# Kernel optimization log

Hardware: AMD Instinct MI355X
Metric: run time of the kernel (lower is better)

## Reference

```python
import jax, jax.numpy as jnp
import numpy as np

N_SRC0, N_FTRS, N_HID, N_CLS = 200000, 128, 1500, 64
E0, E1 = 1600000, 500000
RES0, RES1 = 50000, 10000


def sage_conv(x, src, tgt, res_size, W_root, W_neigh, b):
    # mean aggregation of neighbor (source) features onto the first res_size target nodes
    msg = x[src]                                              # [E, F] gather
    summed = jax.ops.segment_sum(msg, tgt, num_segments=res_size)   # [res, F]
    cnt = jax.ops.segment_sum(jnp.ones((src.shape[0],), x.dtype), tgt, num_segments=res_size)
    mean = summed / jnp.maximum(cnt, 1.0)[:, None]
    return x[:res_size] @ W_root + mean @ W_neigh + b


def setup_inputs() -> dict:
    key = jax.random.key(0)
    ks = jax.random.split(key, 12)
    x = jax.random.normal(ks[0], (N_SRC0, N_FTRS), dtype=jnp.float32)
    edge_src0 = jax.random.randint(ks[1], (E0,), 0, N_SRC0)
    edge_tgt0 = jax.random.randint(ks[2], (E0,), 0, RES0)
    edge_src1 = jax.random.randint(ks[3], (E1,), 0, RES0)
    edge_tgt1 = jax.random.randint(ks[4], (E1,), 0, RES1)
    s1 = 1.0 / np.sqrt(N_FTRS)
    s2 = 1.0 / np.sqrt(N_HID)
    W1_root = jax.random.uniform(ks[5], (N_FTRS, N_HID), jnp.float32, -s1, s1)
    W1_neigh = jax.random.uniform(ks[6], (N_FTRS, N_HID), jnp.float32, -s1, s1)
    b1 = jax.random.uniform(ks[7], (N_HID,), jnp.float32, -s1, s1)
    W2_root = jax.random.uniform(ks[8], (N_HID, N_CLS), jnp.float32, -s2, s2)
    W2_neigh = jax.random.uniform(ks[9], (N_HID, N_CLS), jnp.float32, -s2, s2)
    b2 = jax.random.uniform(ks[10], (N_CLS,), jnp.float32, -s2, s2)
    return {
        "x": x,
        "W1_root": W1_root, "W1_neigh": W1_neigh, "b1": b1,
        "W2_root": W2_root, "W2_neigh": W2_neigh, "b2": b2,
        "edge_src0": edge_src0, "edge_tgt0": edge_tgt0,
        "edge_src1": edge_src1, "edge_tgt1": edge_tgt1,
        "res0": RES0, "res1": RES1,
    }


def reference(x, W1_root, W1_neigh, b1, W2_root, W2_neigh, b2,
              edge_src0, edge_tgt0, edge_src1, edge_tgt1, res0, res1):
    h = sage_conv(x, edge_src0, edge_tgt0, res0, W1_root, W1_neigh, b1)  # [res0, H]
    h = jax.nn.relu(h)
    # dropout p=0.5 is identity in eval mode
    out = sage_conv(h, edge_src1, edge_tgt1, res1, W2_root, W2_neigh, b2)  # [res1, C]
    return jax.nn.log_softmax(out, axis=1)
```

## Files before the change

kernel.cpp:

```cpp
#include <hip/hip_runtime.h>
#include <hip/hip_bf16.h>
#include <cstdint>
#include <cstddef>

#define NSRC   200000
#define NF     128
#define NHID   1500
#define NHIDP  1536
#define NCLS   64
#define E0N    1600000
#define E1N    500000
#define RES0   50000
#define RES1   10000

#define CH     4096
#define NCH0   ((E0N + CH - 1) / CH)
#define NCH1   ((E1N + CH - 1) / CH)
#define NB0    ((RES0 + 255) / 256)
#define NB1    ((RES1 + 255) / 256)

#define PREP_BLOCKS  ((256 * NHIDP + 128 * NHIDP + NHIDP + 255) / 256)
#define COPYX_BLOCKS ((NSRC * NF) / (256 * 8))

typedef __bf16 bf16x8 __attribute__((ext_vector_type(8)));
typedef float  f32x4  __attribute__((ext_vector_type(4)));
typedef unsigned short u16x8 __attribute__((ext_vector_type(8)));
typedef unsigned int u32;
typedef unsigned long long u64;

__device__ __forceinline__ unsigned short f2bf(float f) {
    union { float f; unsigned u; } v; v.f = f;
    unsigned r = v.u + 0x7fffu + ((v.u >> 16) & 1u);
    return (unsigned short)(r >> 16);
}
__device__ __forceinline__ float bf2f(unsigned short b) {
    union { u32 u; float f; } v; v.u = ((u32)b) << 16;
    return v.f;
}

__device__ __forceinline__ u32 cvt_pk_bf16(float lo, float hi) {
    u32 r;
    asm("v_cvt_pk_bf16_f32 %0, %1, %2" : "=v"(r) : "v"(lo), "v"(hi));
    return r;
}

__device__ __forceinline__ void lds_dma16(const void* g, void* lds) {
    __builtin_amdgcn_global_load_lds(
        (const __attribute__((address_space(1))) unsigned int*)g,
        (__attribute__((address_space(3))) unsigned int*)lds, 16, 0, 0);
}

__device__ __forceinline__ void raw_barrier() {
    __asm__ volatile("s_barrier" ::: "memory");
}
__device__ __forceinline__ void wait_vm8() {
    __asm__ volatile("s_waitcnt vmcnt(8)" ::: "memory");
}
__device__ __forceinline__ void wait_vm4() {
    __asm__ volatile("s_waitcnt vmcnt(4)" ::: "memory");
}
__device__ __forceinline__ void wait_vm0() {
    __asm__ volatile("s_waitcnt vmcnt(0)" ::: "memory");
}

__device__ __forceinline__ void p1a_body(const int* __restrict__ tgt, int n,
                                         int nb, u32* __restrict__ H, int c) {
    __shared__ u32 lhist[256];
    int tid = threadIdx.x;
    lhist[tid] = 0;
    __syncthreads();
#pragma unroll
    for (int it = 0; it < CH / 256; ++it) {
        int i = c * CH + it * 256 + tid;
        if (i < n) atomicAdd(&lhist[((u32)tgt[i]) >> 8], 1u);
    }
    __syncthreads();
    if (tid < nb) H[c * nb + tid] = lhist[tid];
}

__global__ __launch_bounds__(256) void setup_kernel(
        const float* __restrict__ x, unsigned short* __restrict__ xbf,
        const float* __restrict__ W1r, const float* __restrict__ W1n,
        const float* __restrict__ b1,
        const float* __restrict__ W2r, const float* __restrict__ W2n,
        unsigned short* __restrict__ WcatT, unsigned short* __restrict__ W2f,
        float* __restrict__ b1e,
        const int* __restrict__ t0, const int* __restrict__ t1,
        u32* __restrict__ H1, u32* __restrict__ H2) {
    int bid = blockIdx.x;
    if (bid < PREP_BLOCKS) {
        int id = bid * 256 + threadIdx.x;
        if (id < 256 * NHIDP) {
            int n = id >> 8, k = id & 255;
            float v = 0.f;
            if (n < NHID) v = (k < NF) ? W1r[k * NHID + n] : W1n[(k - NF) * NHID + n];
            WcatT[n * 256 + k] = f2bf(v);
        } else {
            int id2 = id - 256 * NHIDP;
            if (id2 < 128 * NHIDP) {
                int n = id2 / NHIDP, k = id2 % NHIDP;
                float v = 0.f;
                if (k < NHID) v = (n < 64) ? W2n[k * 64 + n] : W2r[k * 64 + (n - 64)];
                int j = k >> 7, w = k & 127;
                int kk = w >> 5, r = w & 31;
                int hi = r >> 4, qd = (r >> 2) & 3, e = r & 3;
                W2f[(((size_t)(j * 4 + kk) * 128 + n) * 32) + qd * 8 + hi * 4 + e] = f2bf(v);
            } else {
                int c = id2 - 128 * NHIDP;
                if (c < NHIDP) b1e[c] = (c < NHID) ? b1[c] : 0.f;
            }
        }
    } else if (bid < PREP_BLOCKS + COPYX_BLOCKS) {
        size_t i = ((size_t)(bid - PREP_BLOCKS) * 256 + threadIdx.x) * 8;
        const float4* s = (const float4*)(x + i);
        float4 a = s[0], b = s[1];
        u16x8 o;
        o[0] = f2bf(a.x); o[1] = f2bf(a.y); o[2] = f2bf(a.z); o[3] = f2bf(a.w);
        o[4] = f2bf(b.x); o[5] = f2bf(b.y); o[6] = f2bf(b.z); o[7] = f2bf(b.w);
        *(u16x8*)(xbf + i) = o;
    } else {
        int c = bid - (PREP_BLOCKS + COPYX_BLOCKS);
        if (c < NCH0) p1a_body(t0, E0N, NB0, H1, c);
        else          p1a_body(t1, E1N, NB1, H2, c - NCH0);
    }
}

__device__ __forceinline__ void bscan_body(const u32* __restrict__ H,
                                           int nch, int nb, int b,
                                           u32* __restrict__ base_rel,
                                           u32* __restrict__ Bsum) {
    __shared__ u32 part[512];
    int t = threadIdx.x;
    part[t] = (t < nch) ? H[t * nb + b] : 0u;
    __syncthreads();
    for (int d = 1; d < 512; d <<= 1) {
        u32 v = part[t];
        u32 add = (t >= d) ? part[t - d] : 0u;
        __syncthreads();
        part[t] = v + add;
        __syncthreads();
    }
    if (t < nch) base_rel[t * nb + b] = (t == 0) ? 0u : part[t - 1];
    if (t == 0) Bsum[b] = part[nch - 1];
}

__global__ __launch_bounds__(512) void bscan_both_kernel(
        const u32* __restrict__ H1, u32* __restrict__ base1, u32* __restrict__ Bsum1,
        const u32* __restrict__ H2, u32* __restrict__ base2, u32* __restrict__ Bsum2) {
    int b = blockIdx.x;
    if (b < NB0) bscan_body(H1, NCH0, NB0, b, base1, Bsum1);
    else         bscan_body(H2, NCH1, NB1, b - NB0, base2, Bsum2);
}

__global__ __launch_bounds__(256) void boff_kernel(const u32* __restrict__ Bsum1,
                                                   u32* __restrict__ boff1, int nb1,
                                                   const u32* __restrict__ Bsum2,
                                                   u32* __restrict__ boff2, int nb2) {
    const u32* B = blockIdx.x ? Bsum2 : Bsum1;
    u32* O = blockIdx.x ? boff2 : boff1;
    int nb = blockIdx.x ? nb2 : nb1;
    __shared__ u32 part[256];
    int t = threadIdx.x;
    part[t] = (t < nb) ? B[t] : 0u;
    __syncthreads();
    for (int d = 1; d < 256; d <<= 1) {
        u32 v = part[t];
        u32 add = (t >= d) ? part[t - d] : 0u;
        __syncthreads();
        part[t] = v + add;
        __syncthreads();
    }
    if (t < nb) O[t] = (t == 0) ? 0u : part[t - 1];
}

__device__ __forceinline__ void p1b_body(const int* __restrict__ src,
                                         const int* __restrict__ tgt, int n,
                                         int nb, const u32* __restrict__ base_rel,
                                         const u32* __restrict__ boff,
                                         u64* __restrict__ bucketed, int c) {
    __shared__ u32 lcur[256];
    __shared__ u32 lbase[256];
    int tid = threadIdx.x;
    lcur[tid] = 0;
    if (tid < nb) lbase[tid] = base_rel[c * nb + tid] + boff[tid];
    __syncthreads();
#pragma unroll
    for (int it = 0; it < CH / 256; ++it) {
        int i = c * CH + it * 256 + tid;
        if (i < n) {
            u32 t = (u32)tgt[i];
            u32 s = (u32)src[i];
            u32 b = t >> 8;
            u32 r = atomicAdd(&lcur[b], 1u);
            bucketed[lbase[b] + r] = ((u64)t << 32) | (u64)s;
        }
    }
}

__global__ __launch_bounds__(256) void p1b_both_kernel(
        const int* __restrict__ s0, const int* __restrict__ t0,
        const u32* __restrict__ base1, const u32* __restrict__ boff1,
        u64* __restrict__ bkt1,
        const int* __restrict__ s1, const int* __restrict__ t1,
        const u32* __restrict__ base2, const u32* __restrict__ boff2,
        u64* __restrict__ bkt2) {
    int b = blockIdx.x;
    if (b < NCH0) p1b_body(s0, t0, E0N, NB0, base1, boff1, bkt1, b);
    else          p1b_body(s1, t1, E1N, NB1, base2, boff2, bkt2, b - NCH0);
}

__device__ __forceinline__ void p2_body(const u64* __restrict__ bucketed,
                                        const u32* __restrict__ boff,
                                        int nb, int res, int etot,
                                        int* __restrict__ csr,
                                        u32* __restrict__ off_out,
                                        u32* __restrict__ cnt_out, int b) {
    __shared__ u32 lhist[256];
    __shared__ u32 part[256];
    __shared__ u32 cur[256];
    int tid = threadIdx.x;
    u32 start = boff[b];
    u32 end = (b == nb - 1) ? (u32)etot : boff[b + 1];
    u32 count = end - start;
    if (tid < 256) lhist[tid] = 0;
    __syncthreads();
    for (u32 i = tid; i < count; i += 1024) {
        u32 t = (u32)(bucketed[start + i] >> 32);
        atomicAdd(&lhist[t & 255u], 1u);
    }
    __syncthreads();
    if (tid < 256) part[tid] = lhist[tid];
    __syncthreads();
    for (int d = 1; d < 256; d <<= 1) {
        u32 v = (tid < 256) ? part[tid] : 0u;
        u32 add = (tid >= d && tid < 256) ? part[tid - d] : 0u;
        __syncthreads();
        if (tid < 256) part[tid] = v + add;
        __syncthreads();
    }
    if (tid < 256) {
        u32 excl = (tid == 0) ? 0u : part[tid - 1];
        cur[tid] = excl;
        int tg = (b << 8) + tid;
        if (tg < res) {
            off_out[tg] = start + excl;
            cnt_out[tg] = lhist[tid];
        }
    }
    __syncthreads();
    for (u32 i = tid; i < count; i += 1024) {
        u64 pr = bucketed[start + i];
        u32 lt = ((u32)(pr >> 32)) & 255u;
        u32 r = atomicAdd(&cur[lt], 1u);
        csr[start + r] = (int)(u32)pr;
    }
}

__global__ __launch_bounds__(1024) void p2_both_kernel(
        const u64* __restrict__ bkt1, const u32* __restrict__ boff1,
        int* __restrict__ csr1, u32* __restrict__ off1, u32* __restrict__ cnt1,
        const u64* __restrict__ bkt2, const u32* __restrict__ boff2,
        int* __restrict__ csr2, u32* __restrict__ off2, u32* __restrict__ cnt2) {
    int b = blockIdx.x;
    if (b < NB0) p2_body(bkt1, boff1, NB0, RES0, E0N, csr1, off1, cnt1, b);
    else         p2_body(bkt2, boff2, NB1, RES1, E1N, csr2, off2, cnt2, b - NB0);
}

__global__ __launch_bounds__(256) void agg1_csr_kernel(
        const unsigned short* __restrict__ xbf, const int* __restrict__ csr,
        const u32* __restrict__ off, const u32* __restrict__ cnt,
        unsigned short* __restrict__ mean1) {
    int row = blockIdx.x * 4 + (threadIdx.x >> 6);
    int lane = threadIdx.x & 63;
    if (row >= RES0) return;
    int q = lane >> 4, c16 = lane & 15;
    u32 base = off[row], deg = cnt[row];
    float acc[8] = {};
    u32 e = 0;
    for (; e + 16 <= deg; e += 16) {
        int s0 = csr[base + e + q];
        int s1 = csr[base + e + 4 + q];
        int s2 = csr[base + e + 8 + q];
        int s3 = csr[base + e + 12 + q];
        u16x8 v0 = *(const u16x8*)(xbf + (size_t)s0 * NF + c16 * 8);
        u16x8 v1 = *(const u16x8*)(xbf + (size_t)s1 * NF + c16 * 8);
        u16x8 v2 = *(const u16x8*)(xbf + (size_t)s2 * NF + c16 * 8);
        u16x8 v3 = *(const u16x8*)(xbf + (size_t)s3 * NF + c16 * 8);
#pragma unroll
        for (int i = 0; i < 8; ++i)
            acc[i] += (bf2f(v0[i]) + bf2f(v1[i])) + (bf2f(v2[i]) + bf2f(v3[i]));
    }
    for (; e + 8 <= deg; e += 8) {
        int s0 = csr[base + e + q];
        int s1 = csr[base + e + 4 + q];
        u16x8 v0 = *(const u16x8*)(xbf + (size_t)s0 * NF + c16 * 8);
        u16x8 v1 = *(const u16x8*)(xbf + (size_t)s1 * NF + c16 * 8);
#pragma unroll
        for (int i = 0; i < 8; ++i) acc[i] += bf2f(v0[i]) + bf2f(v1[i]);
    }
    for (; e + 4 <= deg; e += 4) {
        int s0 = csr[base + e + q];
        u16x8 v0 = *(const u16x8*)(xbf + (size_t)s0 * NF + c16 * 8);
#pragma unroll
        for (int i = 0; i < 8; ++i) acc[i] += bf2f(v0[i]);
    }
    if (e < deg) {
        bool valid = (e + q) < deg;
        int s0 = csr[base + (valid ? e + q : e)];
        u16x8 v0 = *(const u16x8*)(xbf + (size_t)s0 * NF + c16 * 8);
        if (valid) {
#pragma unroll
            for (int i = 0; i < 8; ++i) acc[i] += bf2f(v0[i]);
        }
    }
#pragma unroll
    for (int i = 0; i < 8; ++i) {
        acc[i] += __shfl_xor(acc[i], 32, 64);
        acc[i] += __shfl_xor(acc[i], 16, 64);
    }
    if (q == 0) {
        float inv = 1.0f / fmaxf((float)deg, 1.0f);
        u16x8 o;
#pragma unroll
        for (int i = 0; i < 8; ++i) o[i] = f2bf(acc[i] * inv);
        *(u16x8*)(mean1 + (size_t)row * NF + c16 * 8) = o;
    }
}

__device__ __forceinline__ void stage_chunk(
        const unsigned short* __restrict__ xbf, const unsigned short* __restrict__ mean1,
        const unsigned short* __restrict__ WcatT, int m0, int j, int kt,
        unsigned short* As, unsigned short* Bs, int wid, int lane) {
    int ksel = kt * 32;
    const unsigned short* srcA = (ksel < 128)
        ? xbf + (size_t)m0 * NF + ksel
        : mean1 + (size_t)m0 * NF + (ksel - 128);
#pragma unroll
    for (int ci = 0; ci < 2; ++ci) {
        int cb = ci * 256 + wid * 64;
        int chunk = cb + lane;
        int n = chunk >> 2, kc = (chunk & 3) ^ (n & 3);
        lds_dma16(srcA + (size_t)n * NF + kc * 8, &As[cb * 8]);
    }
    const unsigned short* srcB = WcatT + (size_t)(j * 128) * 256 + ksel;
#pragma unroll
    for (int ci = 0; ci < 2; ++ci) {
        int cb = ci * 256 + wid * 64;
        int chunk = cb + lane;
        int n = chunk >> 2, kc = (chunk & 3) ^ (n & 3);
        lds_dma16(srcB + (size_t)n * 256 + kc * 8, &Bs[cb * 8]);
    }
}

__global__ __launch_bounds__(256, 2) void fused_gemm_kernel(
        const unsigned short* __restrict__ xbf, const unsigned short* __restrict__ mean1,
        const unsigned short* __restrict__ WcatT, const float* __restrict__ b1e,
        const unsigned short* __restrict__ W2f,
        unsigned short* __restrict__ pnbf, float* __restrict__ root64) {
    __shared__ __align__(16) unsigned short As[4][128 * 32];
    __shared__ __align__(16) unsigned short Bs[4][128 * 32];

    int m0 = blockIdx.x * 128;
    int tid = threadIdx.x;
    int lane = tid & 63, wid = tid >> 6;
    int wm = wid;
    int quad = lane >> 4, l15 = lane & 15;
    const int csw = (quad ^ (l15 & 3)) * 8;

    f32x4 pacc[2][8] = {};

    stage_chunk(xbf, mean1, WcatT, m0, 0, 0, As[0], Bs[0], wid, lane);
    stage_chunk(xbf, mean1, WcatT, m0, 0, 1, As[1], Bs[1], wid, lane);
    stage_chunk(xbf, mean1, WcatT, m0, 0, 2, As[2], Bs[2], wid, lane);

#pragma unroll 1
    for (int jj = 0; jj < 12; ++jj) {
        const int j = jj;
        f32x4 hacc[2][8] = {};
#pragma unroll
        for (int kt = 0; kt < 8; ++kt) {
            const int g = jj * 8 + kt;
            if (g <= 93) wait_vm8();
            else if (g == 94) wait_vm4();
            else wait_vm0();
            raw_barrier();
            if (g + 3 < 96) {
                int g3 = g + 3;
                stage_chunk(xbf, mean1, WcatT, m0, g3 >> 3, g3 & 7,
                            As[g3 & 3], Bs[g3 & 3], wid, lane);
            }
            const unsigned short* Asb = As[g & 3];
            const unsigned short* Bsb = Bs[g & 3];
            bf16x8 a[2], b[8];
#pragma unroll
            for (int mi = 0; mi < 2; ++mi)
                a[mi] = *(const bf16x8*)(&Asb[(wm * 32 + mi * 16 + l15) * 32 + csw]);
#pragma unroll
            for (int ni = 0; ni < 8; ++ni)
                b[ni] = *(const bf16x8*)(&Bsb[(ni * 16 + l15) * 32 + csw]);
            __builtin_amdgcn_s_setprio(1);
#pragma unroll
            for (int mi = 0; mi < 2; ++mi)
#pragma unroll
                for (int ni = 0; ni < 8; ++ni)
                    hacc[mi][ni] = __builtin_amdgcn_mfma_f32_16x16x32_bf16(b[ni], a[mi], hacc[mi][ni], 0, 0, 0);
            __builtin_amdgcn_s_setprio(0);
        }

        u32 a2w[2][4][4];
#pragma unroll
        for (int ni = 0; ni < 8; ++ni) {
            float4 bv = *(const float4*)(b1e + j * 128 + ni * 16 + quad * 4);
#pragma unroll
            for (int mi = 0; mi < 2; ++mi) {
                f32x4 h = hacc[mi][ni];
                float h0 = fmaxf(h[0] + bv.x, 0.f);
                float h1 = fmaxf(h[1] + bv.y, 0.f);
                float h2 = fmaxf(h[2] + bv.z, 0.f);
                float h3 = fmaxf(h[3] + bv.w, 0.f);
                a2w[mi][ni >> 1][(ni & 1) * 2 + 0] = cvt_pk_bf16(h0, h1);
                a2w[mi][ni >> 1][(ni & 1) * 2 + 1] = cvt_pk_bf16(h2, h3);
            }
        }
        __builtin_amdgcn_s_setprio(1);
#pragma unroll
        for (int kk = 0; kk < 4; ++kk) {
            union U { u32 w[4]; bf16x8 v; uint4 q; };
            U A2[2];
#pragma unroll
            for (int mi = 0; mi < 2; ++mi)
#pragma unroll
                for (int w = 0; w < 4; ++w) A2[mi].w[w] = a2w[mi][kk][w];
            const unsigned short* wp =
                W2f + ((size_t)(j * 4 + kk) * 128) * 32 + (size_t)quad * 8;
#pragma unroll
            for (int ni2 = 0; ni2 < 8; ++ni2) {
                U B2;
                B2.q = *(const uint4*)(wp + (size_t)(ni2 * 16 + l15) * 32);
#pragma unroll
                for (int mi = 0; mi < 2; ++mi)
                    pacc[mi][ni2] = __builtin_amdgcn_mfma_f32_16x16x32_bf16(B2.v, A2[mi].v, pacc[mi][ni2], 0, 0, 0);
            }
        }
        __builtin_amdgcn_s_setprio(0);
    }

#pragma unroll
    for (int mi = 0; mi < 2; ++mi) {
        int gr = m0 + wm * 32 + mi * 16 + l15;
        if (gr < RES0) {
#pragma unroll
            for (int ni2 = 0; ni2 < 8; ++ni2) {
                f32x4 s = pacc[mi][ni2];
                if (ni2 < 4) {
                    uint2 o;
                    o.x = (u32)f2bf(s[0]) | ((u32)f2bf(s[1]) << 16);
                    o.y = (u32)f2bf(s[2]) | ((u32)f2bf(s[3]) << 16);
                    *(uint2*)(pnbf + (size_t)gr * 64 + ni2 * 16 + quad * 4) = o;
                } else if (gr < RES1) {
                    *(f32x4*)(root64 + (size_t)gr * 64 + (ni2 - 4) * 16 + quad * 4) = s;
                }
            }
        }
    }
}

__global__ __launch_bounds__(256) void final_csr_kernel(
        const unsigned short* __restrict__ pnbf, const float* __restrict__ root64,
        const int* __restrict__ csr, const u32* __restrict__ off,
        const u32* __restrict__ cnt, const float* __restrict__ b2,
        float* __restrict__ out) {
    int row = blockIdx.x * 4 + (threadIdx.x >> 6);
    int lane = threadIdx.x & 63;
    if (row >= RES1) return;
    int es = lane >> 3, c8 = lane & 7;
    u32 base = off[row], deg = cnt[row];
    float acc[8] = {};
    u32 e = 0;
    for (; e + 8 <= deg; e += 8) {
        int s = csr[base + e + es];
        u16x8 v = *(const u16x8*)(pnbf + (size_t)s * 64 + c8 * 8);
#pragma unroll
        for (int i = 0; i < 8; ++i) acc[i] += bf2f(v[i]);
    }
    if (e < deg) {
        bool valid = (e + es) < deg;
        int s = csr[base + (valid ? e + es : e)];
        u16x8 v = *(const u16x8*)(pnbf + (size_t)s * 64 + c8 * 8);
        if (valid) {
#pragma unroll
            for (int i = 0; i < 8; ++i) acc[i] += bf2f(v[i]);
        }
    }
#pragma unroll
    for (int i = 0; i < 8; ++i) {
        acc[i] += __shfl_xor(acc[i], 32, 64);
        acc[i] += __shfl_xor(acc[i], 16, 64);
        acc[i] += __shfl_xor(acc[i], 8, 64);
    }
    float inv = 1.0f / fmaxf((float)deg, 1.0f);
    float v[8];
    const float* rp = root64 + (size_t)row * 64 + c8 * 8;
#pragma unroll
    for (int i = 0; i < 8; ++i) v[i] = rp[i] + acc[i] * inv + b2[c8 * 8 + i];
    float m = v[0];
#pragma unroll
    for (int i = 1; i < 8; ++i) m = fmaxf(m, v[i]);
    m = fmaxf(m, __shfl_xor(m, 1, 64));
    m = fmaxf(m, __shfl_xor(m, 2, 64));
    m = fmaxf(m, __shfl_xor(m, 4, 64));
    float s = 0.f;
#pragma unroll
    for (int i = 0; i < 8; ++i) s += expf(v[i] - m);
    s += __shfl_xor(s, 1, 64);
    s += __shfl_xor(s, 2, 64);
    s += __shfl_xor(s, 4, 64);
    if (es == 0) {
        float lg = logf(s);
        f32x4 o0, o1;
#pragma unroll
        for (int i = 0; i < 4; ++i) { o0[i] = v[i] - m - lg; o1[i] = v[i + 4] - m - lg; }
        *(f32x4*)(&out[(size_t)row * 64 + c8 * 8])     = o0;
        *(f32x4*)(&out[(size_t)row * 64 + c8 * 8 + 4]) = o1;
    }
}

extern "C" void kernel_launch(void* const* d_in, const int* in_sizes, int n_in,
                              void* d_out, int out_size, void* d_ws, size_t ws_size,
                              hipStream_t stream) {
    const float* x   = (const float*)d_in[0];
    const float* W1r = (const float*)d_in[1];
    const float* W1n = (const float*)d_in[2];
    const float* b1  = (const float*)d_in[3];
    const float* W2r = (const float*)d_in[4];
    const float* W2n = (const float*)d_in[5];
    const float* b2  = (const float*)d_in[6];
    const int* es0 = (const int*)d_in[7];
    const int* et0 = (const int*)d_in[8];
    const int* es1 = (const int*)d_in[9];
    const int* et1 = (const int*)d_in[10];
    float* out = (float*)d_out;

    char* ws = (char*)d_ws;
    size_t off_ = 0;
    auto alloc = [&](size_t bytes) {
        void* ptr = ws + off_;
        off_ = (off_ + bytes + 255) & ~(size_t)255;
        return ptr;
    };
    u64* bkt1  = (u64*)alloc((size_t)E0N * 8);
    u64* bkt2  = (u64*)alloc((size_t)E1N * 8);
    int* csr1  = (int*)alloc((size_t)E0N * 4);
    u32* H1    = (u32*)alloc((size_t)NCH0 * NB0 * 4);
    u32* base1 = (u32*)alloc((size_t)NCH0 * NB0 * 4);
    u32* H2    = (u32*)alloc((size_t)NCH1 * NB1 * 4);
    u32* base2 = (u32*)alloc((size_t)NCH1 * NB1 * 4);
    u32* Bsum1 = (u32*)alloc((size_t)NB0 * 4);
    u32* Bsum2 = (u32*)alloc((size_t)NB1 * 4);
    u32* boff1 = (u32*)alloc((size_t)NB0 * 4);
    u32* boff2 = (u32*)alloc((size_t)NB1 * 4);
    u32* off1  = (u32*)alloc((size_t)RES0 * 4);
    u32* cnt1  = (u32*)alloc((size_t)RES0 * 4);
    int* csr2  = (int*)alloc((size_t)E1N * 4);
    u32* off2  = (u32*)alloc((size_t)RES1 * 4);
    u32* cnt2  = (u32*)alloc((size_t)RES1 * 4);
    unsigned short* xbf    = (unsigned short*)alloc((size_t)NSRC * NF * 2);
    unsigned short* mean1  = (unsigned short*)alloc((size_t)(RES0 + 128) * NF * 2);
    unsigned short* WcatT  = (unsigned short*)alloc((size_t)NHIDP * 256 * 2);
    unsigned short* W2f    = (unsigned short*)alloc((size_t)128 * NHIDP * 2);
    float*          b1e    = (float*)alloc((size_t)NHIDP * 4);
    unsigned short* pnbf   = (unsigned short*)alloc((size_t)RES0 * 64 * 2);
    float*          root64 = (float*)alloc((size_t)RES1 * 64 * 4);

    setup_kernel<<<PREP_BLOCKS + COPYX_BLOCKS + NCH0 + NCH1, 256, 0, stream>>>(
        x, xbf, W1r, W1n, b1, W2r, W2n, WcatT, W2f, b1e, et0, et1, H1, H2);

    bscan_both_kernel<<<NB0 + NB1, 512, 0, stream>>>(H1, base1, Bsum1, H2, base2, Bsum2);
    boff_kernel<<<2, 256, 0, stream>>>(Bsum1, boff1, NB0, Bsum2, boff2, NB1);
    p1b_both_kernel<<<NCH0 + NCH1, 256, 0, stream>>>(
        es0, et0, base1, boff1, bkt1, es1, et1, base2, boff2, bkt2);
    p2_both_kernel<<<NB0 + NB1, 1024, 0, stream>>>(
        bkt1, boff1, csr1, off1, cnt1, bkt2, boff2, csr2, off2, cnt2);

    agg1_csr_kernel<<<(RES0 + 3) / 4, 256, 0, stream>>>(
        xbf, csr1, off1, cnt1, mean1);

    fused_gemm_kernel<<<(RES0 + 127) / 128, 256, 0, stream>>>(
        xbf, mean1, WcatT, b1e, W2f, pnbf, root64);

    final_csr_kernel<<<(RES1 + 3) / 4, 256, 0, stream>>>(
        pnbf, root64, csr2, off2, cnt2, b2, out);
}
```

Baseline: 434.6 us.

## Keep full A tile resident in LDS and load B fragments directly from global

```diff
diff --git a/kernel.cpp b/kernel.cpp
--- a/kernel.cpp
+++ b/kernel.cpp
@@ -50,15 +50,6 @@
         (__attribute__((address_space(3))) unsigned int*)lds, 16, 0, 0);
 }
 
-__device__ __forceinline__ void raw_barrier() {
-    __asm__ volatile("s_barrier" ::: "memory");
-}
-__device__ __forceinline__ void wait_vm8() {
-    __asm__ volatile("s_waitcnt vmcnt(8)" ::: "memory");
-}
-__device__ __forceinline__ void wait_vm4() {
-    __asm__ volatile("s_waitcnt vmcnt(4)" ::: "memory");
-}
 __device__ __forceinline__ void wait_vm0() {
     __asm__ volatile("s_waitcnt vmcnt(0)" ::: "memory");
 }
@@ -327,83 +318,66 @@
     }
 }
 
-__device__ __forceinline__ void stage_chunk(
-        const unsigned short* __restrict__ xbf, const unsigned short* __restrict__ mean1,
-        const unsigned short* __restrict__ WcatT, int m0, int j, int kt,
-        unsigned short* As, unsigned short* Bs, int wid, int lane) {
-    int ksel = kt * 32;
-    const unsigned short* srcA = (ksel < 128)
-        ? xbf + (size_t)m0 * NF + ksel
-        : mean1 + (size_t)m0 * NF + (ksel - 128);
-#pragma unroll
-    for (int ci = 0; ci < 2; ++ci) {
-        int cb = ci * 256 + wid * 64;
-        int chunk = cb + lane;
-        int n = chunk >> 2, kc = (chunk & 3) ^ (n & 3);
-        lds_dma16(srcA + (size_t)n * NF + kc * 8, &As[cb * 8]);
-    }
-    const unsigned short* srcB = WcatT + (size_t)(j * 128) * 256 + ksel;
-#pragma unroll
-    for (int ci = 0; ci < 2; ++ci) {
-        int cb = ci * 256 + wid * 64;
-        int chunk = cb + lane;
-        int n = chunk >> 2, kc = (chunk & 3) ^ (n & 3);
-        lds_dma16(srcB + (size_t)n * 256 + kc * 8, &Bs[cb * 8]);
-    }
-}
-
 __global__ __launch_bounds__(256, 2) void fused_gemm_kernel(
         const unsigned short* __restrict__ xbf, const unsigned short* __restrict__ mean1,
         const unsigned short* __restrict__ WcatT, const float* __restrict__ b1e,
         const unsigned short* __restrict__ W2f,
         unsigned short* __restrict__ pnbf, float* __restrict__ root64) {
-    __shared__ __align__(16) unsigned short As[4][128 * 32];
-    __shared__ __align__(16) unsigned short Bs[4][128 * 32];
+    __shared__ __align__(16) unsigned short Atile[128 * 256];
 
     int m0 = blockIdx.x * 128;
     int tid = threadIdx.x;
     int lane = tid & 63, wid = tid >> 6;
     int wm = wid;
     int quad = lane >> 4, l15 = lane & 15;
-    const int csw = (quad ^ (l15 & 3)) * 8;
+
+#pragma unroll
+    for (int d = 0; d < 16; ++d) {
+        int gd = wid * 16 + d;
+        int r = gd * 2 + (lane >> 5);
+        int kb = ((lane & 31) * 16) ^ ((r & 7) << 4);
+        const unsigned short* src = (kb < 256)
+            ? xbf + (size_t)(m0 + r) * NF + (kb >> 1)
+            : mean1 + (size_t)(m0 + r) * NF + ((kb - 256) >> 1);
+        lds_dma16(src, Atile + gd * 512);
+    }
+    wait_vm0();
+    __syncthreads();
 
     f32x4 pacc[2][8] = {};
-
-    stage_chunk(xbf, mean1, WcatT, m0, 0, 0, As[0], Bs[0], wid, lane);
-    stage_chunk(xbf, mean1, WcatT, m0, 0, 1, As[1], Bs[1], wid, lane);
-    stage_chunk(xbf, mean1, WcatT, m0, 0, 2, As[2], Bs[2], wid, lane);
+    const int r0 = wm * 32 + l15, r1 = r0 + 16;
+    const unsigned short* Bp = WcatT + (size_t)l15 * 256 + quad * 8;
 
 #pragma unroll 1
     for (int jj = 0; jj < 12; ++jj) {
         const int j = jj;
+        const unsigned short* Bj = Bp + (size_t)(j * 128) * 256;
         f32x4 hacc[2][8] = {};
+        bf16x8 bP[2][8];
+#pragma unroll
+        for (int ni = 0; ni < 8; ++ni)
+            bP[0][ni] = *(const bf16x8*)(Bj + (size_t)(ni * 16) * 256);
 #pragma unroll
         for (int kt = 0; kt < 8; ++kt) {
-            const int g = jj * 8 + kt;
-            if (g <= 93) wait_vm8();
-            else if (g == 94) wait_vm4();
-            else wait_vm0();
-            raw_barrier();
-            if (g + 3 < 96) {
-                int g3 = g + 3;
-                stage_chunk(xbf, mean1, WcatT, m0, g3 >> 3, g3 & 7,
-                            As[g3 & 3], Bs[g3 & 3], wid, lane);
+            const int p = kt & 1, q2 = p ^ 1;
+            if (kt < 7) {
+#pragma unroll
+                for (int ni = 0; ni < 8; ++ni)
+                    bP[q2][ni] = *(const bf16x8*)(Bj + (size_t)(ni * 16) * 256 + (kt + 1) * 32);
             }
-            const unsigned short* Asb = As[g & 3];
-            const unsigned short* Bsb = Bs[g & 3];
-            bf16x8 a[2], b[8];
+            bf16x8 a[2];
+            {
+                int kb0 = (kt * 64 + quad * 16) ^ ((r0 & 7) << 4);
+                a[0] = *(const bf16x8*)(Atile + r0 * 256 + (kb0 >> 1));
+                int kb1 = (kt * 64 + quad * 16) ^ ((r1 & 7) << 4);
+                a[1] = *(const bf16x8*)(Atile + r1 * 256 + (kb1 >> 1));
+            }
+            __builtin_amdgcn_s_setprio(1);
 #pragma unroll
             for (int mi = 0; mi < 2; ++mi)
-                a[mi] = *(const bf16x8*)(&Asb[(wm * 32 + mi * 16 + l15) * 32 + csw]);
-#pragma unroll
-            for (int ni = 0; ni < 8; ++ni)
-                b[ni] = *(const bf16x8*)(&Bsb[(ni * 16 + l15) * 32 + csw]);
-            __builtin_amdgcn_s_setprio(1);
-#pragma unroll
-            for (int mi = 0; mi < 2; ++mi)
 #pragma unroll
                 for (int ni = 0; ni < 8; ++ni)
-                    hacc[mi][ni] = __builtin_amdgcn_mfma_f32_16x16x32_bf16(b[ni], a[mi], hacc[mi][ni], 0, 0, 0);
+                    hacc[mi][ni] = __builtin_amdgcn_mfma_f32_16x16x32_bf16(bP[p][ni], a[mi], hacc[mi][ni], 0, 0, 0);
             __builtin_amdgcn_s_setprio(0);
         }
 
```

Measured after the change: 566.4 us. 1.3x slower.
